# Performance work log

Measured on AMD Instinct MI355X. Metric: run time of the kernel, lower is better.

## Reference

```python
import jax, jax.numpy as jnp
import numpy as np

SKS = 3  # small kernel size
PAD = (SKS - 1) // 2
GROUPS = 8


def setup_inputs() -> dict:
    key = jax.random.key(0)
    k1, k2 = jax.random.split(key)
    B, C, H, W = 8, 64, 128, 128
    x = jax.random.normal(k1, (B, C, H, W), dtype=jnp.float32)
    # dynamic per-pixel aggregation weights, shared across Cg within each group
    w = jax.random.normal(k2, (B, GROUPS, 1, SKS * SKS, H, W), dtype=jnp.float32)
    return {"x": x, "w": w}


def reference(x, w):
    # Faithful to: patches = unfold(x, k=3, pad=1).view(B, g, Cg, 9, H, W); (patches * w).sum(3)
    # Implemented as a fused shift-multiply-accumulate over the 9 fixed taps,
    B, C, H, W = x.shape
    g = w.shape[1]
    Cg = C // g
    xp = jnp.pad(x, ((0, 0), (0, 0), (PAD, PAD), (PAD, PAD)))
    xp = xp.reshape(B, g, Cg, H + 2 * PAD, W + 2 * PAD)
    out = jnp.zeros((B, g, Cg, H, W), dtype=x.dtype)
    for k in range(SKS * SKS):  # fixed 9 taps, unrolled at trace time
        ki, kj = divmod(k, SKS)  # unfold orders kernel positions row-major
        out = out + xp[:, :, :, ki:ki + H, kj:kj + W] * w[:, :, :, k]
    return out.reshape(B, C, H, W)
```

## Files before the change

### kernel.cpp

```cpp
#include <hip/hip_runtime.h>
#include <hip/hip_bf16.h>

#define BATCH 8
#define CHN   64
#define GRP   8
#define CG    8
#define HH    128
#define WW    128
#define HW    (HH * WW)

__global__ __launch_bounds__(256, 4) void ska_small_kernel(
    const float* __restrict__ x,
    const float* __restrict__ wgt,
    float* __restrict__ out)
{
    int tid = blockIdx.x * blockDim.x + threadIdx.x;
    int q  = tid & 31;
    int w0 = q * 4;
    int h  = (tid >> 5) & 127;
    int g  = (tid >> 12) & 7;
    int b  = tid >> 15;

    const float* wbase = wgt + ((size_t)(b * GRP + g) * 9) * HW + (size_t)h * WW + w0;
    float4 wk[9];
#pragma unroll
    for (int k = 0; k < 9; ++k) {
        wk[k] = *(const float4*)(wbase + (size_t)k * HW);
    }

    const float m_top = (h > 0)      ? 1.0f : 0.0f;
    const float m_bot = (h < HH - 1) ? 1.0f : 0.0f;
#pragma unroll
    for (int j = 0; j < 3; ++j) {
        wk[j].x     *= m_top; wk[j].y     *= m_top; wk[j].z     *= m_top; wk[j].w     *= m_top;
        wk[6 + j].x *= m_bot; wk[6 + j].y *= m_bot; wk[6 + j].z *= m_bot; wk[6 + j].w *= m_bot;
    }

    const float mL = (q > 0)  ? 1.0f : 0.0f;
    const float mR = (q < 31) ? 1.0f : 0.0f;

    const int hm = (h > 0)      ? h - 1 : h;
    const int hp = (h < HH - 1) ? h + 1 : h;

    const float* xbase = x   + (size_t)(b * CHN + g * CG) * HW + w0;
    float*       obase = out + (size_t)(b * CHN + g * CG) * HW + (size_t)h * WW + w0;

#pragma unroll
    for (int cg = 0; cg < CG; ++cg) {
        const float* xc = xbase + (size_t)cg * HW;
        float4 r0 = *(const float4*)(xc + (size_t)hm * WW);
        float4 r1 = *(const float4*)(xc + (size_t)h  * WW);
        float4 r2 = *(const float4*)(xc + (size_t)hp * WW);

        float xr[3][6];
        xr[0][1] = r0.x; xr[0][2] = r0.y; xr[0][3] = r0.z; xr[0][4] = r0.w;
        xr[1][1] = r1.x; xr[1][2] = r1.y; xr[1][3] = r1.z; xr[1][4] = r1.w;
        xr[2][1] = r2.x; xr[2][2] = r2.y; xr[2][3] = r2.z; xr[2][4] = r2.w;
        xr[0][0] = __shfl_up(r0.w, 1) * mL;
        xr[1][0] = __shfl_up(r1.w, 1) * mL;
        xr[2][0] = __shfl_up(r2.w, 1) * mL;
        xr[0][5] = __shfl_down(r0.x, 1) * mR;
        xr[1][5] = __shfl_down(r1.x, 1) * mR;
        xr[2][5] = __shfl_down(r2.x, 1) * mR;

        float4 acc = make_float4(0.f, 0.f, 0.f, 0.f);
#pragma unroll
        for (int ki = 0; ki < 3; ++ki) {
#pragma unroll
            for (int kj = 0; kj < 3; ++kj) {
                const float4 wv = wk[ki * 3 + kj];
                acc.x = fmaf(xr[ki][0 + kj], wv.x, acc.x);
                acc.y = fmaf(xr[ki][1 + kj], wv.y, acc.y);
                acc.z = fmaf(xr[ki][2 + kj], wv.z, acc.z);
                acc.w = fmaf(xr[ki][3 + kj], wv.w, acc.w);
            }
        }

        *(float4*)(obase + (size_t)cg * HW) = acc;
    }
}

extern "C" void kernel_launch(void* const* d_in, const int* in_sizes, int n_in,
                              void* d_out, int out_size, void* d_ws, size_t ws_size,
                              hipStream_t stream) {
    const float* x = (const float*)d_in[0];
    const float* w = (const float*)d_in[1];
    float* out = (float*)d_out;

    const int total = BATCH * GRP * HH * (WW / 4);
    const int block = 256;
    const int grid = total / block;
    ska_small_kernel<<<grid, block, 0, stream>>>(x, w, out);
}
```

Baseline: 105.6 us.

## Compute two output rows per thread to reuse vertical halo loads

Each thread now produces two adjacent output rows, loading four input rows per channel instead of three per row. This cuts redundant x loads and raises per-thread memory-level parallelism, and the launch bound is relaxed to allow more registers. The total thread count halves, which leaves many CUs underfilled on a wide GPU.

```diff
diff --git a/kernel.cpp b/kernel.cpp
--- a/kernel.cpp
+++ b/kernel.cpp
@@ -9,7 +9,7 @@
 #define WW    128
 #define HW    (HH * WW)
 
-__global__ __launch_bounds__(256, 4) void ska_small_kernel(
+__global__ __launch_bounds__(256, 3) void ska_small_kernel(
     const float* __restrict__ x,
     const float* __restrict__ wgt,
     float* __restrict__ out)
@@ -17,66 +17,81 @@
     int tid = blockIdx.x * blockDim.x + threadIdx.x;
     int q  = tid & 31;
     int w0 = q * 4;
-    int h  = (tid >> 5) & 127;
-    int g  = (tid >> 12) & 7;
-    int b  = tid >> 15;
+    int h2 = (tid >> 5) & 63;
+    int g  = (tid >> 11) & 7;
+    int b  = tid >> 14;
 
-    const float* wbase = wgt + ((size_t)(b * GRP + g) * 9) * HW + (size_t)h * WW + w0;
-    float4 wk[9];
+    const int h0 = h2 * 2;
+    const int h1 = h0 + 1;
+
+    const float* wbase = wgt + ((size_t)(b * GRP + g) * 9) * HW + (size_t)h0 * WW + w0;
+    float4 wk0[9], wk1[9];
 #pragma unroll
     for (int k = 0; k < 9; ++k) {
-        wk[k] = *(const float4*)(wbase + (size_t)k * HW);
+        wk0[k] = *(const float4*)(wbase + (size_t)k * HW);
+        wk1[k] = *(const float4*)(wbase + (size_t)k * HW + WW);
     }
 
-    const float m_top = (h > 0)      ? 1.0f : 0.0f;
-    const float m_bot = (h < HH - 1) ? 1.0f : 0.0f;
+    const float m_top = (h0 > 0)      ? 1.0f : 0.0f;
+    const float m_bot = (h1 < HH - 1) ? 1.0f : 0.0f;
 #pragma unroll
     for (int j = 0; j < 3; ++j) {
-        wk[j].x     *= m_top; wk[j].y     *= m_top; wk[j].z     *= m_top; wk[j].w     *= m_top;
-        wk[6 + j].x *= m_bot; wk[6 + j].y *= m_bot; wk[6 + j].z *= m_bot; wk[6 + j].w *= m_bot;
+        wk0[j].x     *= m_top; wk0[j].y     *= m_top; wk0[j].z     *= m_top; wk0[j].w     *= m_top;
+        wk1[6 + j].x *= m_bot; wk1[6 + j].y *= m_bot; wk1[6 + j].z *= m_bot; wk1[6 + j].w *= m_bot;
     }
 
     const float mL = (q > 0)  ? 1.0f : 0.0f;
     const float mR = (q < 31) ? 1.0f : 0.0f;
 
-    const int hm = (h > 0)      ? h - 1 : h;
-    const int hp = (h < HH - 1) ? h + 1 : h;
+    const int hm = (h0 > 0)      ? h0 - 1 : h0;
+    const int hp = (h1 < HH - 1) ? h1 + 1 : h1;
 
     const float* xbase = x   + (size_t)(b * CHN + g * CG) * HW + w0;
-    float*       obase = out + (size_t)(b * CHN + g * CG) * HW + (size_t)h * WW + w0;
+    float*       obase = out + (size_t)(b * CHN + g * CG) * HW + (size_t)h0 * WW + w0;
 
 #pragma unroll
     for (int cg = 0; cg < CG; ++cg) {
         const float* xc = xbase + (size_t)cg * HW;
-        float4 r0 = *(const float4*)(xc + (size_t)hm * WW);
-        float4 r1 = *(const float4*)(xc + (size_t)h  * WW);
-        float4 r2 = *(const float4*)(xc + (size_t)hp * WW);
+        float4 rm = *(const float4*)(xc + (size_t)hm * WW);
+        float4 r0 = *(const float4*)(xc + (size_t)h0 * WW);
+        float4 r1 = *(const float4*)(xc + (size_t)h1 * WW);
+        float4 rp = *(const float4*)(xc + (size_t)hp * WW);
 
-        float xr[3][6];
-        xr[0][1] = r0.x; xr[0][2] = r0.y; xr[0][3] = r0.z; xr[0][4] = r0.w;
-        xr[1][1] = r1.x; xr[1][2] = r1.y; xr[1][3] = r1.z; xr[1][4] = r1.w;
-        xr[2][1] = r2.x; xr[2][2] = r2.y; xr[2][3] = r2.z; xr[2][4] = r2.w;
-        xr[0][0] = __shfl_up(r0.w, 1) * mL;
-        xr[1][0] = __shfl_up(r1.w, 1) * mL;
-        xr[2][0] = __shfl_up(r2.w, 1) * mL;
-        xr[0][5] = __shfl_down(r0.x, 1) * mR;
-        xr[1][5] = __shfl_down(r1.x, 1) * mR;
-        xr[2][5] = __shfl_down(r2.x, 1) * mR;
+        float win[4][6];
+        win[0][1] = rm.x; win[0][2] = rm.y; win[0][3] = rm.z; win[0][4] = rm.w;
+        win[1][1] = r0.x; win[1][2] = r0.y; win[1][3] = r0.z; win[1][4] = r0.w;
+        win[2][1] = r1.x; win[2][2] = r1.y; win[2][3] = r1.z; win[2][4] = r1.w;
+        win[3][1] = rp.x; win[3][2] = rp.y; win[3][3] = rp.z; win[3][4] = rp.w;
+        win[0][0] = __shfl_up(rm.w, 1) * mL;
+        win[1][0] = __shfl_up(r0.w, 1) * mL;
+        win[2][0] = __shfl_up(r1.w, 1) * mL;
+        win[3][0] = __shfl_up(rp.w, 1) * mL;
+        win[0][5] = __shfl_down(rm.x, 1) * mR;
+        win[1][5] = __shfl_down(r0.x, 1) * mR;
+        win[2][5] = __shfl_down(r1.x, 1) * mR;
+        win[3][5] = __shfl_down(rp.x, 1) * mR;
 
-        float4 acc = make_float4(0.f, 0.f, 0.f, 0.f);
+        float4 acc0 = make_float4(0.f, 0.f, 0.f, 0.f);
+        float4 acc1 = make_float4(0.f, 0.f, 0.f, 0.f);
 #pragma unroll
         for (int ki = 0; ki < 3; ++ki) {
 #pragma unroll
             for (int kj = 0; kj < 3; ++kj) {
-                const float4 wv = wk[ki * 3 + kj];
-                acc.x = fmaf(xr[ki][0 + kj], wv.x, acc.x);
-                acc.y = fmaf(xr[ki][1 + kj], wv.y, acc.y);
-                acc.z = fmaf(xr[ki][2 + kj], wv.z, acc.z);
-                acc.w = fmaf(xr[ki][3 + kj], wv.w, acc.w);
+                const float4 wv0 = wk0[ki * 3 + kj];
+                const float4 wv1 = wk1[ki * 3 + kj];
+                acc0.x = fmaf(win[ki    ][0 + kj], wv0.x, acc0.x);
+                acc0.y = fmaf(win[ki    ][1 + kj], wv0.y, acc0.y);
+                acc0.z = fmaf(win[ki    ][2 + kj], wv0.z, acc0.z);
+                acc0.w = fmaf(win[ki    ][3 + kj], wv0.w, acc0.w);
+                acc1.x = fmaf(win[ki + 1][0 + kj], wv1.x, acc1.x);
+                acc1.y = fmaf(win[ki + 1][1 + kj], wv1.y, acc1.y);
+                acc1.z = fmaf(win[ki + 1][2 + kj], wv1.z, acc1.z);
+                acc1.w = fmaf(win[ki + 1][3 + kj], wv1.w, acc1.w);
             }
         }
 
-        *(float4*)(obase + (size_t)cg * HW) = acc;
+        *(float4*)(obase + (size_t)cg * HW)      = acc0;
+        *(float4*)(obase + (size_t)cg * HW + WW) = acc1;
     }
 }
 
@@ -87,7 +102,7 @@
     const float* w = (const float*)d_in[1];
     float* out = (float*)d_out;
 
-    const int total = BATCH * GRP * HH * (WW / 4);
+    const int total = BATCH * GRP * (HH / 2) * (WW / 4);
     const int block = 256;
     const int grid = total / block;
     ska_small_kernel<<<grid, block, 0, stream>>>(x, w, out);
```

After: 106.2 us, median of 2. Within noise of the previous version (+0.6%).
